# Performance work log

Hardware: AMD Instinct MI355X
Metric: run time of the kernel (lower is better)

## Reference

```python
import jax, jax.numpy as jnp
import numpy as np

EMB = 1024
HEADS = EMB // 64  # 16, head_dim = 64


def setup_inputs() -> dict:
    key = jax.random.key(0)
    ks = jax.random.split(key, 9)
    a, m, t, e = 4, 2048, 2048, EMB
    s = 1.0 / np.sqrt(e)
    return {
        "q": jax.random.normal(ks[0], (a, m, e), jnp.float32),
        "k": jax.random.normal(ks[1], (a, t, e), jnp.float32),
        "v": jax.random.normal(ks[2], (a, t, e), jnp.float32),
        "Wq": jax.random.normal(ks[3], (e, e), jnp.float32) * s,
        "bq": jnp.zeros((e,), jnp.float32),
        "Wk": jax.random.normal(ks[4], (e, e), jnp.float32) * s,
        "bk": jnp.zeros((e,), jnp.float32),
        "Wv": jax.random.normal(ks[5], (e, e), jnp.float32) * s,
        "bv": jnp.zeros((e,), jnp.float32),
    }


def reference(q, k, v, Wq, bq, Wk, bk, Wv, bv):
    a, m, e = q.shape
    t = k.shape[1]
    h = HEADS
    # linear projections (torch Linear: x @ W.T + b)
    qp = (q @ Wq.T + bq).reshape(a, m, h, -1).transpose(0, 2, 1, 3)  # [a,h,m,c]
    kp = (k @ Wk.T + bk).reshape(a, t, h, -1).transpose(0, 2, 1, 3)  # [a,h,t,c]
    vp = (v @ Wv.T + bv).reshape(a, t, h, -1).transpose(0, 2, 1, 3)  # [a,h,t,c]
    # NOTE: original forward never applies self.scale — unscaled QK^T (faithful)
    dots = jnp.einsum('ahmc,ahtc->ahmt', qp, kp)
    attn = jax.nn.softmax(dots, axis=-1)
    out = jnp.einsum('ahmt,ahtc->ahmc', attn, vp)
    return out.transpose(0, 2, 1, 3).reshape(a, m, e)
```

## Files before the change

kernel.cpp:

```cpp
#include <hip/hip_runtime.h>
#include <hip/hip_bf16.h>
#include <hip/hip_fp16.h>

using half8  = __attribute__((ext_vector_type(8))) _Float16;
using float4v = __attribute__((ext_vector_type(4))) float;
using f32x16 = __attribute__((ext_vector_type(16))) float;
typedef unsigned int uint;

#define A_DIM 4
#define M_DIM 2048
#define E_DIM 1024
#define H_DIM 16
#define C_DIM 64
#define PLANE (M_DIM * C_DIM)
#define PROJ_ELEMS (A_DIM * H_DIM * PLANE)
#define LOG2E 1.44269504088896f

#define GLOAD_LDS16(g, l) __builtin_amdgcn_global_load_lds( \
    (const __attribute__((address_space(1))) void*)(g), \
    (__attribute__((address_space(3))) void*)(l), 16, 0, 0)

#if __has_builtin(__builtin_amdgcn_exp2f)
#define EXP2F(x) __builtin_amdgcn_exp2f(x)
#else
#define EXP2F(x) exp2f(x)
#endif

static __device__ __forceinline__ uint pk16(float a, float b) {
    auto r = __builtin_amdgcn_cvt_pkrtz(a, b);
    return __builtin_bit_cast(uint, r);
}

static __device__ __forceinline__ half8 ldsfrag_cvt(const float* base, int row, int colbyte) {
    const char* b = (const char*)base;
    int off = row * 256 + (colbyte ^ ((row & 7) << 4));
    float4v x0 = *reinterpret_cast<const float4v*>(b + off);
    float4v x1 = *reinterpret_cast<const float4v*>(b + (off ^ 16));
    union { uint u[4]; half8 v; } r;
    r.u[0] = pk16(x0[0], x0[1]);
    r.u[1] = pk16(x0[2], x0[3]);
    r.u[2] = pk16(x1[0], x1[1]);
    r.u[3] = pk16(x1[2], x1[3]);
    return r.v;
}

template<int MODE>
__global__ __launch_bounds__(256, 2)
void proj_kernel(const float* __restrict__ X, const float* __restrict__ W,
                 const float* __restrict__ bias, _Float16* __restrict__ out)
{
    __shared__ float ldsA[128 * 64];
    __shared__ float ldsB[128 * 64];

    const int tid  = threadIdx.x;
    const int lane = tid & 63;
    const int wave = tid >> 6;
    const int wr = wave >> 1, wc = wave & 1;
    const int g = lane >> 4, r16 = lane & 15;
    const int R0 = blockIdx.x * 128;
    const int C0 = blockIdx.y * 128;

    float4v acc[4][4];
#pragma unroll
    for (int i = 0; i < 4; i++)
#pragma unroll
        for (int j = 0; j < 4; j++) acc[i][j] = {0.f, 0.f, 0.f, 0.f};

    for (int k0 = 0; k0 < E_DIM; k0 += 64) {
        __syncthreads();
#pragma unroll
        for (int i = 0; i < 8; i++) {
            int seg  = i * 256 + tid;
            int row  = seg >> 4;
            int swzo = ((seg & 15) * 16) ^ ((row & 7) << 4);
            const char* asrc = (const char*)&X[(size_t)(R0 + row) * E_DIM + k0] + swzo;
            const char* bsrc = (const char*)&W[(size_t)(C0 + row) * E_DIM + k0] + swzo;
            GLOAD_LDS16(asrc, &ldsA[seg * 4]);
            GLOAD_LDS16(bsrc, &ldsB[seg * 4]);
        }
        __syncthreads();

#pragma unroll
        for (int kc = 0; kc < 2; kc++) {
            const int cb = kc * 128 + g * 32;
            half8 af[4], bf[4];
#pragma unroll
            for (int mi = 0; mi < 4; mi++)
                af[mi] = ldsfrag_cvt(ldsA, wr * 64 + mi * 16 + r16, cb);
#pragma unroll
            for (int ni = 0; ni < 4; ni++)
                bf[ni] = ldsfrag_cvt(ldsB, wc * 64 + ni * 16 + r16, cb);
#pragma unroll
            for (int mi = 0; mi < 4; mi++)
#pragma unroll
                for (int ni = 0; ni < 4; ni++)
                    acc[mi][ni] = __builtin_amdgcn_mfma_f32_16x16x32_f16(af[mi], bf[ni], acc[mi][ni], 0, 0, 0);
        }
    }

#pragma unroll
    for (int mi = 0; mi < 4; mi++) {
#pragma unroll
        for (int ni = 0; ni < 4; ni++) {
            const int jb = C0 + wc * 64 + ni * 16 + r16;
            const int h  = jb >> 6;
            const int cc = jb & 63;
            const float bv = bias[jb];
            if (MODE == 0) {
#pragma unroll
                for (int reg = 0; reg < 4; reg++) {
                    int b = R0 + wr * 64 + mi * 16 + g * 4 + reg;
                    float val = acc[mi][ni][reg] + bv;
                    size_t o = (size_t)((b >> 11) * H_DIM + h) * PLANE + (size_t)(b & (M_DIM - 1)) * C_DIM + cc;
                    out[o] = (_Float16)val;
                }
            } else {
                int b0 = R0 + wr * 64 + mi * 16 + g * 4;
                union { uint u[2]; _Float16 h[4]; } pkv;
                pkv.u[0] = pk16(acc[mi][ni][0] + bv, acc[mi][ni][1] + bv);
                pkv.u[1] = pk16(acc[mi][ni][2] + bv, acc[mi][ni][3] + bv);
                size_t o = (size_t)((b0 >> 11) * H_DIM + h) * PLANE + (size_t)cc * M_DIM + (b0 & (M_DIM - 1));
                *reinterpret_cast<uint*>(&out[o]) = pkv.u[0];
                *reinterpret_cast<uint*>(&out[o] + 2) = pkv.u[1];
            }
        }
    }
}

__global__ __launch_bounds__(256, 4)
void flash_kernel(const _Float16* __restrict__ qp, const _Float16* __restrict__ kp,
                  const _Float16* __restrict__ vt, float* __restrict__ out)
{
    __shared__ _Float16 smem[2][2][4096];

    const int tid  = threadIdx.x;
    const int lane = tid & 63;
    const int wave = tid >> 6;
    const int l31  = lane & 31;
    const int hi   = lane >> 5;

    const int bid = blockIdx.x;
    const int wg  = ((bid & 7) << 7) | (bid >> 3);
    const int plane_i = wg >> 4;
    const int qt      = wg & 15;
    const size_t plane = (size_t)plane_i * PLANE;
    const int q0 = qt * 128 + wave * 32;

    const int srow  = tid >> 3;
    const int lincb = (tid & 7) * 16;
    const int scb   = lincb ^ ((srow & 7) << 4);

    half8 qf[4];
#pragma unroll
    for (int ch = 0; ch < 4; ch++)
        qf[ch] = *reinterpret_cast<const half8*>(&qp[plane + (size_t)(q0 + l31) * C_DIM + ch * 16 + hi * 8]);

    f32x16 o0, o1;
#pragma unroll
    for (int i = 0; i < 16; i++) { o0[i] = 0.f; o1[i] = 0.f; }
    float m = -INFINITY, l = 0.f;

    auto stage = [&](int buf, int t0) {
#pragma unroll
        for (int i = 0; i < 2; i++) {
            int row = srow + 32 * i;
            const char* ksrc = (const char*)&kp[plane + (size_t)(t0 + row) * C_DIM] + scb;
            const char* vsrc = (const char*)&vt[plane + (size_t)row * M_DIM + t0] + scb;
            GLOAD_LDS16(ksrc, &smem[buf][0][tid * 8 + 2048 * i]);
            GLOAD_LDS16(vsrc, &smem[buf][1][tid * 8 + 2048 * i]);
        }
    };

    stage(0, 0);

    for (int it = 0; it < M_DIM / 64; ++it) {
        __syncthreads();
        if (it + 1 < M_DIM / 64) stage((it + 1) & 1, (it + 1) * 64);
        const int cur = it & 1;
        const char* kbase = (const char*)smem[cur][0];
        const char* vbase = (const char*)smem[cur][1];

#pragma unroll
        for (int st = 0; st < 2; ++st) {
            const int krow = st * 32 + l31;
            const int kswz = (krow & 7) << 4;
            f32x16 s;
#pragma unroll
            for (int i = 0; i < 16; i++) s[i] = 0.f;
            __builtin_amdgcn_s_setprio(1);
#pragma unroll
            for (int ch = 0; ch < 4; ch++) {
                int cb = (ch * 32 + hi * 16) ^ kswz;
                half8 kf = *reinterpret_cast<const half8*>(kbase + krow * 128 + cb);
                s = __builtin_amdgcn_mfma_f32_32x32x16_f16(kf, qf[ch], s, 0, 0, 0);
            }
            __builtin_amdgcn_s_setprio(0);

            float a0 = fmaxf(fmaxf(s[0],  s[1]),  s[2]);
            float a1 = fmaxf(fmaxf(s[3],  s[4]),  s[5]);
            float a2 = fmaxf(fmaxf(s[6],  s[7]),  s[8]);
            float a3 = fmaxf(fmaxf(s[9],  s[10]), s[11]);
            float a4 = fmaxf(fmaxf(s[12], s[13]), s[14]);
            float pm = fmaxf(fmaxf(fmaxf(a0, a1), a2),
                             fmaxf(fmaxf(a3, a4), s[15]));
            pm = fmaxf(pm, __shfl_xor(pm, 32));
            if (!__all(pm <= m + 8.f)) {
                float mnew = fmaxf(m, pm);
                float sc = EXP2F((m - mnew) * LOG2E);
                m = mnew; l *= sc;
                o0 *= sc; o1 *= sc;
            }
            const float mK = m * LOG2E;
            float p[16];
#pragma unroll
            for (int r = 0; r < 16; r++) p[r] = EXP2F(fmaf(s[r], LOG2E, -mK));
            float t0a = (p[0] + p[1]) + (p[2] + p[3]);
            float t1a = (p[4] + p[5]) + (p[6] + p[7]);
            float t2a = (p[8] + p[9]) + (p[10] + p[11]);
            float t3a = (p[12] + p[13]) + (p[14] + p[15]);
            l += (t0a + t1a) + (t2a + t3a);

            half8 pf[2];
#pragma unroll
            for (int c0 = 0; c0 < 2; c0++) {
                uint ua0 = pk16(p[8 * c0 + 0], p[8 * c0 + 1]);
                uint ua1 = pk16(p[8 * c0 + 2], p[8 * c0 + 3]);
                uint ub0 = pk16(p[8 * c0 + 4], p[8 * c0 + 5]);
                uint ub1 = pk16(p[8 * c0 + 6], p[8 * c0 + 7]);
                uint v0 = hi ? ua0 : ub0;
                uint v1 = hi ? ua1 : ub1;
                uint y0 = (uint)__shfl_xor((int)v0, 32);
                uint y1 = (uint)__shfl_xor((int)v1, 32);
                union { uint u[4]; half8 v; } pu;
                pu.u[0] = hi ? y0 : ua0;
                pu.u[1] = hi ? y1 : ua1;
                pu.u[2] = hi ? ub0 : y0;
                pu.u[3] = hi ? ub1 : y1;
                pf[c0] = pu.v;
            }

            __builtin_amdgcn_s_setprio(1);
#pragma unroll
            for (int db = 0; db < 2; db++) {
                const int vrow = db * 32 + l31;
                const int vswz = (vrow & 7) << 4;
#pragma unroll
                for (int c0 = 0; c0 < 2; c0++) {
                    int cb = (st * 64 + c0 * 32 + hi * 16) ^ vswz;
                    half8 vf = *reinterpret_cast<const half8*>(vbase + vrow * 128 + cb);
                    if (db == 0) o0 = __builtin_amdgcn_mfma_f32_32x32x16_f16(vf, pf[c0], o0, 0, 0, 0);
                    else         o1 = __builtin_amdgcn_mfma_f32_32x32x16_f16(vf, pf[c0], o1, 0, 0, 0);
                }
            }
            __builtin_amdgcn_s_setprio(0);
        }
    }

    const int aa = plane_i >> 4;
    const int hh = plane_i & 15;
    const float lt = l + __shfl_xor(l, 32);
    const float inv = 1.f / lt;
    float* obase = out + ((size_t)(aa * M_DIM + q0 + l31)) * E_DIM + hh * C_DIM;
#pragma unroll
    for (int db = 0; db < 2; db++) {
#pragma unroll
        for (int g4 = 0; g4 < 4; g4++) {
            float4v w;
#pragma unroll
            for (int j = 0; j < 4; j++) w[j] = (db ? o1[4 * g4 + j] : o0[4 * g4 + j]) * inv;
            int d0 = db * 32 + 8 * g4 + 4 * hi;
            *reinterpret_cast<float4v*>(obase + d0) = w;
        }
    }
}

extern "C" void kernel_launch(void* const* d_in, const int* in_sizes, int n_in,
                              void* d_out, int out_size, void* d_ws, size_t ws_size,
                              hipStream_t stream)
{
    const float* q  = (const float*)d_in[0];
    const float* k  = (const float*)d_in[1];
    const float* v  = (const float*)d_in[2];
    const float* Wq = (const float*)d_in[3];
    const float* bq = (const float*)d_in[4];
    const float* Wk = (const float*)d_in[5];
    const float* bk = (const float*)d_in[6];
    const float* Wv = (const float*)d_in[7];
    const float* bv = (const float*)d_in[8];
    float* out = (float*)d_out;

    _Float16* qp = (_Float16*)d_ws;
    _Float16* kp = qp + PROJ_ELEMS;
    _Float16* vt = kp + PROJ_ELEMS;

    dim3 pg(64, 8), pb(256);
    hipLaunchKernelGGL((proj_kernel<0>), pg, pb, 0, stream, q, Wq, bq, qp);
    hipLaunchKernelGGL((proj_kernel<0>), pg, pb, 0, stream, k, Wk, bk, kp);
    hipLaunchKernelGGL((proj_kernel<1>), pg, pb, 0, stream, v, Wv, bv, vt);
    hipLaunchKernelGGL(flash_kernel, dim3(A_DIM * H_DIM * (M_DIM / 128)), dim3(256), 0, stream, qp, kp, vt, out);
}
```

Before: 206.8 us.

## Merge QKV projections into one launch with double-buffered LDS and XCD-aware tiling

Replaces three separate projection launches with one 3D grid launch that picks q/k/v by blockIdx.y. The K loop now uses 32-wide steps with double-buffered LDS, so global-to-LDS loads for the next step overlap MFMA work on the current one. Block IDs are remapped so that each XCD gets a contiguous group of row tiles, which is meant to improve L2 reuse of X rows. It also reduces launch overhead and tail effects. In exchange it adds a runtime branch on the transposed store path, and it uses the same total LDS per block.

Result: slower. 212.0 us (+2.5%).

```diff
diff --git a/kernel.cpp b/kernel.cpp
--- a/kernel.cpp
+++ b/kernel.cpp
@@ -31,9 +31,9 @@
     return __builtin_bit_cast(uint, r);
 }
 
-static __device__ __forceinline__ half8 ldsfrag_cvt(const float* base, int row, int colbyte) {
+static __device__ __forceinline__ half8 ldsfrag_cvt32(const float* base, int row, int gb) {
     const char* b = (const char*)base;
-    int off = row * 256 + (colbyte ^ ((row & 7) << 4));
+    int off = row * 128 + (gb ^ ((row & 7) << 4));
     float4v x0 = *reinterpret_cast<const float4v*>(b + off);
     float4v x1 = *reinterpret_cast<const float4v*>(b + (off ^ 16));
     union { uint u[4]; half8 v; } r;
@@ -44,58 +44,77 @@
     return r.v;
 }
 
-template<int MODE>
 __global__ __launch_bounds__(256, 2)
-void proj_kernel(const float* __restrict__ X, const float* __restrict__ W,
-                 const float* __restrict__ bias, _Float16* __restrict__ out)
+void proj_kernel(const float* __restrict__ q, const float* __restrict__ k,
+                 const float* __restrict__ v,
+                 const float* __restrict__ Wq, const float* __restrict__ Wk,
+                 const float* __restrict__ Wv,
+                 const float* __restrict__ bq, const float* __restrict__ bk,
+                 const float* __restrict__ bv,
+                 _Float16* __restrict__ qp, _Float16* __restrict__ kp,
+                 _Float16* __restrict__ vt)
 {
-    __shared__ float ldsA[128 * 64];
-    __shared__ float ldsB[128 * 64];
+    __shared__ float ldsA[2][128 * 32];
+    __shared__ float ldsB[2][128 * 32];
+
+    const int z = blockIdx.y;
+    const float* X    = (z == 0) ? q  : (z == 1) ? k  : v;
+    const float* W    = (z == 0) ? Wq : (z == 1) ? Wk : Wv;
+    const float* bias = (z == 0) ? bq : (z == 1) ? bk : bv;
+    _Float16* out     = (z == 0) ? qp : (z == 1) ? kp : vt;
+    const bool TR = (z == 2);
+
+    const int bid = blockIdx.x;
+    const int xcd = bid & 7;
+    const int idx = bid >> 3;
+    const int R0 = (xcd * 8 + (idx >> 3)) * 128;
+    const int C0 = (idx & 7) * 128;
 
     const int tid  = threadIdx.x;
     const int lane = tid & 63;
     const int wave = tid >> 6;
     const int wr = wave >> 1, wc = wave & 1;
     const int g = lane >> 4, r16 = lane & 15;
-    const int R0 = blockIdx.x * 128;
-    const int C0 = blockIdx.y * 128;
-
-    float4v acc[4][4];
-#pragma unroll
-    for (int i = 0; i < 4; i++)
-#pragma unroll
-        for (int j = 0; j < 4; j++) acc[i][j] = {0.f, 0.f, 0.f, 0.f};
-
-    for (int k0 = 0; k0 < E_DIM; k0 += 64) {
-        __syncthreads();
-#pragma unroll
-        for (int i = 0; i < 8; i++) {
+
+    auto stage = [&](int buf, int k0) {
+#pragma unroll
+        for (int i = 0; i < 4; i++) {
             int seg  = i * 256 + tid;
-            int row  = seg >> 4;
-            int swzo = ((seg & 15) * 16) ^ ((row & 7) << 4);
+            int row  = seg >> 3;
+            int swzo = ((seg & 7) * 16) ^ ((row & 7) << 4);
             const char* asrc = (const char*)&X[(size_t)(R0 + row) * E_DIM + k0] + swzo;
             const char* bsrc = (const char*)&W[(size_t)(C0 + row) * E_DIM + k0] + swzo;
-            GLOAD_LDS16(asrc, &ldsA[seg * 4]);
-            GLOAD_LDS16(bsrc, &ldsB[seg * 4]);
-        }
+            GLOAD_LDS16(asrc, &ldsA[buf][seg * 4]);
+            GLOAD_LDS16(bsrc, &ldsB[buf][seg * 4]);
+        }
+    };
+
+    float4v acc[4][4];
+#pragma unroll
+    for (int i = 0; i < 4; i++)
+#pragma unroll
+        for (int j = 0; j < 4; j++) acc[i][j] = {0.f, 0.f, 0.f, 0.f};
+
+    stage(0, 0);
+
+    for (int it = 0; it < E_DIM / 32; ++it) {
         __syncthreads();
-
-#pragma unroll
-        for (int kc = 0; kc < 2; kc++) {
-            const int cb = kc * 128 + g * 32;
-            half8 af[4], bf[4];
-#pragma unroll
-            for (int mi = 0; mi < 4; mi++)
-                af[mi] = ldsfrag_cvt(ldsA, wr * 64 + mi * 16 + r16, cb);
+        if (it + 1 < E_DIM / 32) stage((it + 1) & 1, (it + 1) * 32);
+        const float* A = ldsA[it & 1];
+        const float* B = ldsB[it & 1];
+
+        half8 af[4], bf[4];
+#pragma unroll
+        for (int mi = 0; mi < 4; mi++)
+            af[mi] = ldsfrag_cvt32(A, wr * 64 + mi * 16 + r16, g * 32);
+#pragma unroll
+        for (int ni = 0; ni < 4; ni++)
+            bf[ni] = ldsfrag_cvt32(B, wc * 64 + ni * 16 + r16, g * 32);
+#pragma unroll
+        for (int mi = 0; mi < 4; mi++)
 #pragma unroll
             for (int ni = 0; ni < 4; ni++)
-                bf[ni] = ldsfrag_cvt(ldsB, wc * 64 + ni * 16 + r16, cb);
-#pragma unroll
-            for (int mi = 0; mi < 4; mi++)
-#pragma unroll
-                for (int ni = 0; ni < 4; ni++)
-                    acc[mi][ni] = __builtin_amdgcn_mfma_f32_16x16x32_f16(af[mi], bf[ni], acc[mi][ni], 0, 0, 0);
-        }
+                acc[mi][ni] = __builtin_amdgcn_mfma_f32_16x16x32_f16(af[mi], bf[ni], acc[mi][ni], 0, 0, 0);
     }
 
 #pragma unroll
@@ -106,7 +125,7 @@
             const int h  = jb >> 6;
             const int cc = jb & 63;
             const float bv = bias[jb];
-            if (MODE == 0) {
+            if (!TR) {
 #pragma unroll
                 for (int reg = 0; reg < 4; reg++) {
                     int b = R0 + wr * 64 + mi * 16 + g * 4 + reg;
@@ -116,12 +135,11 @@
                 }
             } else {
                 int b0 = R0 + wr * 64 + mi * 16 + g * 4;
-                union { uint u[2]; _Float16 h[4]; } pkv;
-                pkv.u[0] = pk16(acc[mi][ni][0] + bv, acc[mi][ni][1] + bv);
-                pkv.u[1] = pk16(acc[mi][ni][2] + bv, acc[mi][ni][3] + bv);
+                uint u0 = pk16(acc[mi][ni][0] + bv, acc[mi][ni][1] + bv);
+                uint u1 = pk16(acc[mi][ni][2] + bv, acc[mi][ni][3] + bv);
                 size_t o = (size_t)((b0 >> 11) * H_DIM + h) * PLANE + (size_t)cc * M_DIM + (b0 & (M_DIM - 1));
-                *reinterpret_cast<uint*>(&out[o]) = pkv.u[0];
-                *reinterpret_cast<uint*>(&out[o] + 2) = pkv.u[1];
+                *reinterpret_cast<uint*>(&out[o]) = u0;
+                *reinterpret_cast<uint*>(&out[o] + 2) = u1;
             }
         }
     }
@@ -293,9 +311,7 @@
     _Float16* kp = qp + PROJ_ELEMS;
     _Float16* vt = kp + PROJ_ELEMS;
 
-    dim3 pg(64, 8), pb(256);
-    hipLaunchKernelGGL((proj_kernel<0>), pg, pb, 0, stream, q, Wq, bq, qp);
-    hipLaunchKernelGGL((proj_kernel<0>), pg, pb, 0, stream, k, Wk, bk, kp);
-    hipLaunchKernelGGL((proj_kernel<1>), pg, pb, 0, stream, v, Wv, bv, vt);
+    hipLaunchKernelGGL(proj_kernel, dim3(512, 3), dim3(256), 0, stream,
+                       q, k, v, Wq, Wk, Wv, bq, bk, bv, qp, kp, vt);
     hipLaunchKernelGGL(flash_kernel, dim3(A_DIM * H_DIM * (M_DIM / 128)), dim3(256), 0, stream, qp, kp, vt, out);
 }
```

## Double-buffer projection GEMM LDS tiles and use 512-thread blocks

Applied to the files above, without the earlier changes.

The projection GEMM now double-buffers its A and B tiles in LDS, issuing the next k-slice's global-to-LDS loads before computing the current one, so only one barrier is needed per iteration. The block grows to 512 threads (8 waves), each wave owning a 32x64 sub-tile instead of 64x64. The aim is to hide global load latency behind the MFMA work. In exchange LDS use doubles to 128KB per block, which forces one block per CU and lowers MFMA work per fragment load, since the A/B fragment conversions are amortized over fewer MFMAs.

Measured after the change: 270.9 us. 1.31x slower.

```diff
diff --git a/kernel.cpp b/kernel.cpp
--- a/kernel.cpp
+++ b/kernel.cpp
@@ -31,9 +31,9 @@
     return __builtin_bit_cast(uint, r);
 }
 
-static __device__ __forceinline__ half8 ldsfrag_cvt(const float* base, int row, int colbyte) {
+static __device__ __forceinline__ half8 ldsfrag_cvt256(const float* base, int row, int gb) {
     const char* b = (const char*)base;
-    int off = row * 256 + (colbyte ^ ((row & 7) << 4));
+    int off = row * 256 + (gb ^ ((row & 7) << 4));
     float4v x0 = *reinterpret_cast<const float4v*>(b + off);
     float4v x1 = *reinterpret_cast<const float4v*>(b + (off ^ 16));
     union { uint u[4]; half8 v; } r;
@@ -45,53 +45,61 @@
 }
 
 template<int MODE>
-__global__ __launch_bounds__(256, 2)
+__global__ __launch_bounds__(512, 1)
 void proj_kernel(const float* __restrict__ X, const float* __restrict__ W,
                  const float* __restrict__ bias, _Float16* __restrict__ out)
 {
-    __shared__ float ldsA[128 * 64];
-    __shared__ float ldsB[128 * 64];
+    __shared__ float ldsA[2][128 * 64];
+    __shared__ float ldsB[2][128 * 64];
 
     const int tid  = threadIdx.x;
     const int lane = tid & 63;
     const int wave = tid >> 6;
-    const int wr = wave >> 1, wc = wave & 1;
+    const int wr = wave >> 1;
+    const int wcl = wave & 1;
     const int g = lane >> 4, r16 = lane & 15;
     const int R0 = blockIdx.x * 128;
     const int C0 = blockIdx.y * 128;
 
-    float4v acc[4][4];
-#pragma unroll
-    for (int i = 0; i < 4; i++)
-#pragma unroll
-        for (int j = 0; j < 4; j++) acc[i][j] = {0.f, 0.f, 0.f, 0.f};
-
-    for (int k0 = 0; k0 < E_DIM; k0 += 64) {
-        __syncthreads();
-#pragma unroll
-        for (int i = 0; i < 8; i++) {
-            int seg  = i * 256 + tid;
-            int row  = seg >> 4;
-            int swzo = ((seg & 15) * 16) ^ ((row & 7) << 4);
+    auto stage = [&](int buf, int k0 ) {
+#pragma unroll
+        for (int i = 0; i < 4; i++) {
+            int s    = i * 512 + tid;
+            int row  = s >> 4;
+            int swzo = ((s & 15) * 16) ^ ((row & 7) << 4);
             const char* asrc = (const char*)&X[(size_t)(R0 + row) * E_DIM + k0] + swzo;
             const char* bsrc = (const char*)&W[(size_t)(C0 + row) * E_DIM + k0] + swzo;
-            GLOAD_LDS16(asrc, &ldsA[seg * 4]);
-            GLOAD_LDS16(bsrc, &ldsB[seg * 4]);
-        }
+            GLOAD_LDS16(asrc, &ldsA[buf][s * 4]);
+            GLOAD_LDS16(bsrc, &ldsB[buf][s * 4]);
+        }
+    };
+
+    float4v acc[2][4];
+#pragma unroll
+    for (int i = 0; i < 2; i++)
+#pragma unroll
+        for (int j = 0; j < 4; j++) acc[i][j] = {0.f, 0.f, 0.f, 0.f};
+
+    stage(0, 0);
+
+    for (int it = 0; it < E_DIM / 64; ++it) {
         __syncthreads();
+        if (it + 1 < E_DIM / 64) stage((it + 1) & 1, (it + 1) * 64);
+        const float* A = ldsA[it & 1];
+        const float* B = ldsB[it & 1];
 
 #pragma unroll
         for (int kc = 0; kc < 2; kc++) {
-            const int cb = kc * 128 + g * 32;
-            half8 af[4], bf[4];
-#pragma unroll
-            for (int mi = 0; mi < 4; mi++)
-                af[mi] = ldsfrag_cvt(ldsA, wr * 64 + mi * 16 + r16, cb);
+            const int gb = kc * 128 + g * 32;
+            half8 af[2], bf[4];
+#pragma unroll
+            for (int mi = 0; mi < 2; mi++)
+                af[mi] = ldsfrag_cvt256(A, wr * 32 + mi * 16 + r16, gb);
 #pragma unroll
             for (int ni = 0; ni < 4; ni++)
-                bf[ni] = ldsfrag_cvt(ldsB, wc * 64 + ni * 16 + r16, cb);
-#pragma unroll
-            for (int mi = 0; mi < 4; mi++)
+                bf[ni] = ldsfrag_cvt256(B, wcl * 64 + ni * 16 + r16, gb);
+#pragma unroll
+            for (int mi = 0; mi < 2; mi++)
 #pragma unroll
                 for (int ni = 0; ni < 4; ni++)
                     acc[mi][ni] = __builtin_amdgcn_mfma_f32_16x16x32_f16(af[mi], bf[ni], acc[mi][ni], 0, 0, 0);
@@ -99,29 +107,28 @@
     }
 
 #pragma unroll
-    for (int mi = 0; mi < 4; mi++) {
+    for (int mi = 0; mi < 2; mi++) {
 #pragma unroll
         for (int ni = 0; ni < 4; ni++) {
-            const int jb = C0 + wc * 64 + ni * 16 + r16;
+            const int jb = C0 + wcl * 64 + ni * 16 + r16;
             const int h  = jb >> 6;
             const int cc = jb & 63;
             const float bv = bias[jb];
             if (MODE == 0) {
 #pragma unroll
                 for (int reg = 0; reg < 4; reg++) {
-                    int b = R0 + wr * 64 + mi * 16 + g * 4 + reg;
+                    int b = R0 + wr * 32 + mi * 16 + g * 4 + reg;
                     float val = acc[mi][ni][reg] + bv;
                     size_t o = (size_t)((b >> 11) * H_DIM + h) * PLANE + (size_t)(b & (M_DIM - 1)) * C_DIM + cc;
                     out[o] = (_Float16)val;
                 }
             } else {
-                int b0 = R0 + wr * 64 + mi * 16 + g * 4;
-                union { uint u[2]; _Float16 h[4]; } pkv;
-                pkv.u[0] = pk16(acc[mi][ni][0] + bv, acc[mi][ni][1] + bv);
-                pkv.u[1] = pk16(acc[mi][ni][2] + bv, acc[mi][ni][3] + bv);
+                int b0 = R0 + wr * 32 + mi * 16 + g * 4;
+                uint u0 = pk16(acc[mi][ni][0] + bv, acc[mi][ni][1] + bv);
+                uint u1 = pk16(acc[mi][ni][2] + bv, acc[mi][ni][3] + bv);
                 size_t o = (size_t)((b0 >> 11) * H_DIM + h) * PLANE + (size_t)cc * M_DIM + (b0 & (M_DIM - 1));
-                *reinterpret_cast<uint*>(&out[o]) = pkv.u[0];
-                *reinterpret_cast<uint*>(&out[o] + 2) = pkv.u[1];
+                *reinterpret_cast<uint*>(&out[o]) = u0;
+                *reinterpret_cast<uint*>(&out[o] + 2) = u1;
             }
         }
     }
@@ -293,7 +300,7 @@
     _Float16* kp = qp + PROJ_ELEMS;
     _Float16* vt = kp + PROJ_ELEMS;
 
-    dim3 pg(64, 8), pb(256);
+    dim3 pg(64, 8), pb(512);
     hipLaunchKernelGGL((proj_kernel<0>), pg, pb, 0, stream, q, Wq, bq, qp);
     hipLaunchKernelGGL((proj_kernel<0>), pg, pb, 0, stream, k, Wk, bk, kp);
     hipLaunchKernelGGL((proj_kernel<1>), pg, pb, 0, stream, v, Wv, bv, vt);
```
